# Performance work log

Hardware: AMD Instinct MI355X
Metric: run time of the kernel (lower is better)

Reference implementation:

```python
import jax, jax.numpy as jnp
import numpy as np

NEG_INF = -1e6  # d2l masked_softmax fill value


def setup_inputs() -> dict:
    key = jax.random.key(0)
    kq, kk, kv, kl = jax.random.split(key, 4)
    n, s, d = 32, 2048, 64
    queries = jax.random.normal(kq, (n, s, d), dtype=jnp.float32)
    keys = jax.random.normal(kk, (n, s, d), dtype=jnp.float32)
    values = jax.random.normal(kv, (n, s, d), dtype=jnp.float32)
    valid_lens = jax.random.randint(kl, (n,), 1, s + 1, dtype=jnp.int32)
    return {"queries": queries, "keys": keys, "values": values, "valid_lens": valid_lens}


def reference(queries, keys, values, valid_lens):
    d = queries.shape[-1]
    # scores: [n, q, k]
    scores = jnp.einsum("nqd,nkd->nqk", queries, keys) / jnp.sqrt(jnp.float32(d))
    kv_len = scores.shape[-1]
    # masked_softmax: positions >= valid_len get NEG_INF before softmax
    mask = jnp.arange(kv_len, dtype=jnp.int32)[None, None, :] < valid_lens[:, None, None]
    scores = jnp.where(mask, scores, NEG_INF)
    attn = jax.nn.softmax(scores, axis=-1)
    # dropout rate 0.0 (inference) -> identity
    return jnp.einsum("nqk,nkd->nqd", attn, values)
```

## Files before the change

### kernel.cpp

```cpp
#include <hip/hip_runtime.h>
#include <hip/hip_bf16.h>


typedef short bf16x8 __attribute__((ext_vector_type(8)));
typedef float f32x4  __attribute__((ext_vector_type(4)));
typedef float f32x16 __attribute__((ext_vector_type(16)));
typedef unsigned int u32;
typedef u32 u32x2 __attribute__((ext_vector_type(2)));
typedef u32 u32x4 __attribute__((ext_vector_type(4)));

#define SEQ 2048
#define DH 64
#define BK 64
#define LDSP 72
#define SCLQ 0.18033688011112042f

static __device__ __forceinline__ short f2bf(float f) {
    unsigned u = __float_as_uint(f);
    return (short)((u + 0x7FFFu + ((u >> 16) & 1u)) >> 16);
}
static __device__ __forceinline__ u32 pk2bf(float lo, float hi) {
    __hip_bfloat162 h = __float22bfloat162_rn(float2{lo, hi});
    return *(u32*)&h;
}
static __device__ __forceinline__ void pl32swap(u32& a, u32& b) {
    asm volatile("v_permlane32_swap_b32 %0, %1" : "+v"(a), "+v"(b));
}

__global__ __launch_bounds__(256, 4)
void prepass(const float* __restrict__ K, const float* __restrict__ V,
             short* __restrict__ Kbf, short* __restrict__ Vt)
{
    __shared__ short T[DH][LDSP];

    const int tid  = threadIdx.x;
    const int wave = tid >> 6;
    const int lane = tid & 63;
    const int b  = blockIdx.x & 31;
    const int kt = blockIdx.x >> 5;
    const int k0 = kt * BK;
    const size_t bo = (size_t)b * SEQ * DH;

    const float* Ks = K + bo + (size_t)k0 * DH;
    u32* Kd = (u32*)(Kbf + bo + (size_t)k0 * DH);
    #pragma unroll
    for (int h = 0; h < 2; ++h) {
        const int c2 = tid + h * 256;
        f32x4 a = *(const f32x4*)(Ks + c2 * 8);
        f32x4 c = *(const f32x4*)(Ks + c2 * 8 + 4);
        u32x4 o;
        o[0] = pk2bf(a[0], a[1]); o[1] = pk2bf(a[2], a[3]);
        o[2] = pk2bf(c[0], c[1]); o[3] = pk2bf(c[2], c[3]);
        *(u32x4*)(Kd + c2 * 4) = o;
    }

    #pragma unroll
    for (int h = 0; h < 2; ++h) {
        const int d0 = wave * 8 + h * 32;
        const float* src = V + bo + (size_t)(k0 + lane) * DH + d0;
        f32x4 va = *(const f32x4*)(src);
        f32x4 vb = *(const f32x4*)(src + 4);
        #pragma unroll
        for (int j = 0; j < 4; ++j) {
            T[d0 + j][lane]     = f2bf(va[j]);
            T[d0 + 4 + j][lane] = f2bf(vb[j]);
        }
    }
    __syncthreads();

    short* Vd = Vt + (size_t)b * DH * SEQ;
    #pragma unroll
    for (int h = 0; h < 2; ++h) {
        const int c2 = tid + h * 256;
        const int d  = c2 >> 3;
        const int kc = (c2 & 7) * 8;
        *(bf16x8*)(Vd + (size_t)d * SEQ + k0 + kc) = *(const bf16x8*)(&T[d][kc]);
    }
}

template <bool PRE>
__global__ __launch_bounds__(256, 2)
void attn_fwd(const float* __restrict__ Q,
              const float* __restrict__ Kf, const float* __restrict__ Vf,
              const short* __restrict__ Kbf, const short* __restrict__ Vtg,
              const int* __restrict__ VL, float* __restrict__ O)
{
    __shared__ __align__(16) short Klds[2][BK][LDSP];
    __shared__ __align__(16) short Vt[2][DH][LDSP];
    __shared__ int Rsort[32];

    const int tid  = threadIdx.x;
    const int wave = tid >> 6;
    const int lane = tid & 63;
    const int qg   = wave & 1;
    const int kg   = wave >> 1;
    const int hi   = lane >> 5;
    const int l31  = lane & 31;
    const int pt   = (qg << 6) | lane;

    if (tid < 32) {
        const int nv = (VL[tid] + BK - 1) >> 6;
        int rank = 0;
        for (int jj = 0; jj < 32; ++jj) {
            const int nj = (VL[jj] + BK - 1) >> 6;
            rank += (nj > nv) || (nj == nv && jj < tid);
        }
        Rsort[rank] = tid;
    }
    __syncthreads();

    const int jb = blockIdx.x & 255;
    const int sl = blockIdx.x >> 8;
    const int c8 = jb >> 5;
    const int qt = jb & 31;
    const int rk = (sl == 0) ? c8 : (sl == 1) ? (15 - c8)
                 : (sl == 2) ? (16 + c8) : (31 - c8);
    const int b  = Rsort[rk];

    const int vl   = VL[b];
    const int nkt  = (vl + BK - 1) >> 6;
    const int nkt2 = (nkt + 1) >> 1;

    const size_t bo = (size_t)b * SEQ * DH;
    const short* Kb = Kbf + bo;
    const short* Vb = Vtg + (size_t)b * DH * SEQ;
    const float* Kb32 = Kf + bo;
    const float* Vb32 = Vf + bo;

    const int qrow = qt * 64 + qg * 32 + l31;
    bf16x8 aq[4];
    {
        const float* qp = Q + bo + (size_t)qrow * DH + hi * 8;
        #pragma unroll
        for (int st = 0; st < 4; ++st) {
            f32x4 a = *(const f32x4*)(qp + st * 16);
            f32x4 c = *(const f32x4*)(qp + st * 16 + 4);
            #pragma unroll
            for (int j = 0; j < 4; ++j) {
                aq[st][j]     = f2bf(a[j] * SCLQ);
                aq[st][j + 4] = f2bf(c[j] * SCLQ);
            }
        }
    }

    bf16x8 ones;
    #pragma unroll
    for (int j = 0; j < 8; ++j) ones[j] = (short)0x3F80;

    f32x16 oacc0, oacc1, lacc;
    #pragma unroll
    for (int i = 0; i < 16; ++i) { oacc0[i] = 0.f; oacc1[i] = 0.f; lacc[i] = 0.f; }

    bf16x8 kpre[4], vpre[4];
    if (PRE && kg < nkt) {
        const size_t k0p = (size_t)kg * BK;
        #pragma unroll
        for (int h = 0; h < 4; ++h) {
            const int c = pt + h * 128;
            kpre[h] = *(const bf16x8*)(Kb + k0p * DH + c * 8);
            vpre[h] = *(const bf16x8*)(Vb + (size_t)(c >> 3) * SEQ + k0p + (c & 7) * 8);
        }
    }

    int kt = kg;
    for (int it = 0; it < nkt2; ++it, kt += 2) {
        const bool act = (kt < nkt);
        const int k0 = kt * BK;

        if (act) {
            if (PRE) {
                #pragma unroll
                for (int h = 0; h < 4; ++h) {
                    const int c = pt + h * 128;
                    *(bf16x8*)(&Klds[kg][c >> 3][(c & 7) * 8]) = kpre[h];
                    *(bf16x8*)(&Vt[kg][c >> 3][(c & 7) * 8])   = vpre[h];
                }
            } else {
                #pragma unroll
                for (int h = 0; h < 4; ++h) {
                    const int c = pt + h * 128;
                    const float* ks = Kb32 + (size_t)(k0 + (c >> 3)) * DH + (c & 7) * 8;
                    f32x4 a = *(const f32x4*)ks;
                    f32x4 d = *(const f32x4*)(ks + 4);
                    u32x4 o;
                    o[0] = pk2bf(a[0], a[1]); o[1] = pk2bf(a[2], a[3]);
                    o[2] = pk2bf(d[0], d[1]); o[3] = pk2bf(d[2], d[3]);
                    *(u32x4*)(&Klds[kg][c >> 3][(c & 7) * 8]) = o;
                }
                #pragma unroll
                for (int h = 0; h < 4; ++h) {
                    const int d0 = qg * 32 + h * 8;
                    const float* vs = Vb32 + (size_t)(k0 + lane) * DH + d0;
                    f32x4 a = *(const f32x4*)vs;
                    f32x4 d = *(const f32x4*)(vs + 4);
                    #pragma unroll
                    for (int j = 0; j < 4; ++j) {
                        Vt[kg][d0 + j][lane]     = f2bf(a[j]);
                        Vt[kg][d0 + 4 + j][lane] = f2bf(d[j]);
                    }
                }
            }
        }
        __syncthreads();

        if (PRE && kt + 2 < nkt) {
            const size_t kn = (size_t)(k0 + 2 * BK);
            #pragma unroll
            for (int h = 0; h < 4; ++h) {
                const int c = pt + h * 128;
                kpre[h] = *(const bf16x8*)(Kb + kn * DH + c * 8);
                vpre[h] = *(const bf16x8*)(Vb + (size_t)(c >> 3) * SEQ + kn + (c & 7) * 8);
            }
        }

        if (act) {
            __builtin_amdgcn_s_setprio(1);
            f32x16 s0, s1;
            #pragma unroll
            for (int i = 0; i < 16; ++i) { s0[i] = 0.f; s1[i] = 0.f; }
            #pragma unroll
            for (int st = 0; st < 4; ++st) {
                bf16x8 a0 = *(const bf16x8*)(&Klds[kg][l31][st * 16 + hi * 8]);
                bf16x8 a1 = *(const bf16x8*)(&Klds[kg][32 + l31][st * 16 + hi * 8]);
                s0 = __builtin_amdgcn_mfma_f32_32x32x16_bf16(a0, aq[st], s0, 0, 0, 0);
                s1 = __builtin_amdgcn_mfma_f32_32x32x16_bf16(a1, aq[st], s1, 0, 0, 0);
            }

            if (k0 + BK <= vl) {
                #pragma unroll
                for (int r = 0; r < 16; ++r) {
                    s0[r] = __builtin_amdgcn_exp2f(s0[r]);
                    s1[r] = __builtin_amdgcn_exp2f(s1[r]);
                }
            } else {
                #pragma unroll
                for (int r = 0; r < 16; ++r) {
                    const int krow = k0 + (r & 3) + 8 * (r >> 2) + 4 * hi;
                    s0[r] = (krow < vl)      ? __builtin_amdgcn_exp2f(s0[r]) : 0.f;
                    s1[r] = (krow + 32 < vl) ? __builtin_amdgcn_exp2f(s1[r]) : 0.f;
                }
            }

            u32 pk0[8], pk1[8];
            #pragma unroll
            for (int i = 0; i < 8; ++i) {
                pk0[i] = pk2bf(s0[2 * i], s0[2 * i + 1]);
                pk1[i] = pk2bf(s1[2 * i], s1[2 * i + 1]);
            }

            bf16x8 ap[4];
            #pragma unroll
            for (int t = 0; t < 2; ++t) {
                u32 x0 = pk0[4 * t], x1 = pk0[4 * t + 1];
                u32 x2 = pk0[4 * t + 2], x3 = pk0[4 * t + 3];
                pl32swap(x0, x2); pl32swap(x1, x3);
                u32x4 w; w[0] = x0; w[1] = x1; w[2] = x2; w[3] = x3;
                ap[t] = *(bf16x8*)&w;
                u32 y0 = pk1[4 * t], y1 = pk1[4 * t + 1];
                u32 y2 = pk1[4 * t + 2], y3 = pk1[4 * t + 3];
                pl32swap(y0, y2); pl32swap(y1, y3);
                u32x4 v; v[0] = y0; v[1] = y1; v[2] = y2; v[3] = y3;
                ap[2 + t] = *(bf16x8*)&v;
            }

            #pragma unroll
            for (int ks = 0; ks < 4; ++ks) {
                lacc = __builtin_amdgcn_mfma_f32_32x32x16_bf16(ap[ks], ones, lacc, 0, 0, 0);
                bf16x8 b0 = *(const bf16x8*)(&Vt[kg][l31][ks * 16 + hi * 8]);
                bf16x8 b1 = *(const bf16x8*)(&Vt[kg][32 + l31][ks * 16 + hi * 8]);
                oacc0 = __builtin_amdgcn_mfma_f32_32x32x16_bf16(ap[ks], b0, oacc0, 0, 0, 0);
                oacc1 = __builtin_amdgcn_mfma_f32_32x32x16_bf16(ap[ks], b1, oacc1, 0, 0, 0);
            }
            __builtin_amdgcn_s_setprio(0);
        }
        __syncthreads();
    }

    float* red = (qg ? (float*)&Vt[0][0][0] : (float*)&Klds[0][0][0]) + lane * 52;
    if (kg == 1) {
        *(f32x16*)(red)      = oacc0;
        *(f32x16*)(red + 16) = oacc1;
        *(f32x16*)(red + 32) = lacc;
    }
    __syncthreads();
    if (kg == 0) {
        f32x16 po0 = *(const f32x16*)(red);
        f32x16 po1 = *(const f32x16*)(red + 16);
        f32x16 pl  = *(const f32x16*)(red + 32);
        #pragma unroll
        for (int r = 0; r < 16; ++r) {
            const float inv = 1.0f / (lacc[r] + pl[r]);
            const int row = qt * 64 + qg * 32 + (r & 3) + 8 * (r >> 2) + 4 * hi;
            O[bo + (size_t)row * DH + l31]      = (oacc0[r] + po0[r]) * inv;
            O[bo + (size_t)row * DH + 32 + l31] = (oacc1[r] + po1[r]) * inv;
        }
    }
}

extern "C" void kernel_launch(void* const* d_in, const int* in_sizes, int n_in,
                              void* d_out, int out_size, void* d_ws, size_t ws_size,
                              hipStream_t stream) {
    const float* Q  = (const float*)d_in[0];
    const float* K  = (const float*)d_in[1];
    const float* V  = (const float*)d_in[2];
    const int*   VL = (const int*)d_in[3];
    float* O = (float*)d_out;

    const size_t nel = (size_t)32 * SEQ * DH;
    const size_t need = 2 * nel * sizeof(short);
    if (ws_size >= need) {
        short* Kbf = (short*)d_ws;
        short* Vt  = Kbf + nel;
        prepass<<<dim3(1024), dim3(256), 0, stream>>>(K, V, Kbf, Vt);
        attn_fwd<true><<<dim3(1024), dim3(256), 0, stream>>>(Q, K, V, Kbf, Vt, VL, O);
    } else {
        attn_fwd<false><<<dim3(1024), dim3(256), 0, stream>>>(Q, K, V, nullptr, nullptr, VL, O);
    }
}
```

Baseline: 132.1 us.

## Pre-swizzle K/V into MFMA fragment layout and load directly from global, drop LDS staging

New measurement: 134.7 us. 2.0% more time.

```diff
diff --git a/kernel.cpp b/kernel.cpp
--- a/kernel.cpp
+++ b/kernel.cpp
@@ -6,13 +6,14 @@
 typedef float f32x4  __attribute__((ext_vector_type(4)));
 typedef float f32x16 __attribute__((ext_vector_type(16)));
 typedef unsigned int u32;
-typedef u32 u32x2 __attribute__((ext_vector_type(2)));
 typedef u32 u32x4 __attribute__((ext_vector_type(4)));
 
 #define SEQ 2048
 #define DH 64
 #define BK 64
 #define LDSP 72
+#define FRAG 512
+#define TILE_SH 4096
 #define SCLQ 0.18033688011112042f
 
 static __device__ __forceinline__ short f2bf(float f) {
@@ -29,7 +30,7 @@
 
 __global__ __launch_bounds__(256, 4)
 void prepass(const float* __restrict__ K, const float* __restrict__ V,
-             short* __restrict__ Kbf, short* __restrict__ Vt)
+             short* __restrict__ KF, short* __restrict__ VF)
 {
     __shared__ short T[DH][LDSP];
 
@@ -37,21 +38,25 @@
     const int wave = tid >> 6;
     const int lane = tid & 63;
     const int b  = blockIdx.x & 31;
-    const int kt = blockIdx.x >> 5;
-    const int k0 = kt * BK;
+    const int t  = blockIdx.x >> 5;
+    const int k0 = t * BK;
     const size_t bo = (size_t)b * SEQ * DH;
+    const size_t tb = (size_t)(b * 32 + t) * TILE_SH;
 
     const float* Ks = K + bo + (size_t)k0 * DH;
-    u32* Kd = (u32*)(Kbf + bo + (size_t)k0 * DH);
+    short* Kd = KF + tb;
     #pragma unroll
     for (int h = 0; h < 2; ++h) {
-        const int c2 = tid + h * 256;
-        f32x4 a = *(const f32x4*)(Ks + c2 * 8);
-        f32x4 c = *(const f32x4*)(Ks + c2 * 8 + 4);
+        const int c = tid + h * 256;
+        const int f = c >> 6;
+        const int row = (f & 1) * 32 + (c & 31);
+        const int col = (f >> 1) * 16 + ((c >> 5) & 1) * 8;
+        f32x4 a = *(const f32x4*)(Ks + row * DH + col);
+        f32x4 d = *(const f32x4*)(Ks + row * DH + col + 4);
         u32x4 o;
         o[0] = pk2bf(a[0], a[1]); o[1] = pk2bf(a[2], a[3]);
-        o[2] = pk2bf(c[0], c[1]); o[3] = pk2bf(c[2], c[3]);
-        *(u32x4*)(Kd + c2 * 4) = o;
+        o[2] = pk2bf(d[0], d[1]); o[3] = pk2bf(d[2], d[3]);
+        *(u32x4*)(Kd + c * 8) = o;
     }
 
     #pragma unroll
@@ -68,35 +73,34 @@
     }
     __syncthreads();
 
-    short* Vd = Vt + (size_t)b * DH * SEQ;
+    short* Vd = VF + tb;
     #pragma unroll
     for (int h = 0; h < 2; ++h) {
-        const int c2 = tid + h * 256;
-        const int d  = c2 >> 3;
-        const int kc = (c2 & 7) * 8;
-        *(bf16x8*)(Vd + (size_t)d * SEQ + k0 + kc) = *(const bf16x8*)(&T[d][kc]);
+        const int c = tid + h * 256;
+        const int f = c >> 6;
+        const int trow = (f & 1) * 32 + (c & 31);
+        const int tcol = (f >> 1) * 16 + ((c >> 5) & 1) * 8;
+        *(bf16x8*)(Vd + c * 8) = *(const bf16x8*)(&T[trow][tcol]);
     }
 }
 
 template <bool PRE>
-__global__ __launch_bounds__(256, 2)
+__global__ __launch_bounds__(256, 4)
 void attn_fwd(const float* __restrict__ Q,
               const float* __restrict__ Kf, const float* __restrict__ Vf,
-              const short* __restrict__ Kbf, const short* __restrict__ Vtg,
+              const short* __restrict__ KF, const short* __restrict__ VF,
               const int* __restrict__ VL, float* __restrict__ O)
 {
-    __shared__ __align__(16) short Klds[2][BK][LDSP];
-    __shared__ __align__(16) short Vt[2][DH][LDSP];
+    __shared__ __align__(16) float Red[2][64][44];
     __shared__ int Rsort[32];
 
     const int tid  = threadIdx.x;
     const int wave = tid >> 6;
     const int lane = tid & 63;
     const int qg   = wave & 1;
-    const int kg   = wave >> 1;
+    const int pg   = wave >> 1;
     const int hi   = lane >> 5;
     const int l31  = lane & 31;
-    const int pt   = (qg << 6) | lane;
 
     if (tid < 32) {
         const int nv = (VL[tid] + BK - 1) >> 6;
@@ -115,17 +119,17 @@
     const int qt = jb & 31;
     const int rk = (sl == 0) ? c8 : (sl == 1) ? (15 - c8)
                  : (sl == 2) ? (16 + c8) : (31 - c8);
-    const int b  = Rsort[rk];
-
-    const int vl   = VL[b];
-    const int nkt  = (vl + BK - 1) >> 6;
-    const int nkt2 = (nkt + 1) >> 1;
+    int b = Rsort[rk];
+    b = __builtin_amdgcn_readfirstlane(b);
+
+    const int vl  = __builtin_amdgcn_readfirstlane(VL[b]);
+    const int nkt = (vl + BK - 1) >> 6;
 
     const size_t bo = (size_t)b * SEQ * DH;
-    const short* Kb = Kbf + bo;
-    const short* Vb = Vtg + (size_t)b * DH * SEQ;
-    const float* Kb32 = Kf + bo;
-    const float* Vb32 = Vf + bo;
+    const short* KFb = KF + (size_t)b * 32 * TILE_SH;
+    const short* VFb = VF + (size_t)b * 32 * TILE_SH;
+    const float* Kf32 = Kf + bo;
+    const float* Vf32 = Vf + bo;
 
     const int qrow = qt * 64 + qg * 32 + l31;
     bf16x8 aq[4];
@@ -143,156 +147,154 @@
         }
     }
 
-    bf16x8 ones;
+    f32x16 oacc0, oacc1;
     #pragma unroll
-    for (int j = 0; j < 8; ++j) ones[j] = (short)0x3F80;
-
-    f32x16 oacc0, oacc1, lacc;
-    #pragma unroll
-    for (int i = 0; i < 16; ++i) { oacc0[i] = 0.f; oacc1[i] = 0.f; lacc[i] = 0.f; }
-
-    bf16x8 kpre[4], vpre[4];
-    if (PRE && kg < nkt) {
-        const size_t k0p = (size_t)kg * BK;
-        #pragma unroll
-        for (int h = 0; h < 4; ++h) {
-            const int c = pt + h * 128;
-            kpre[h] = *(const bf16x8*)(Kb + k0p * DH + c * 8);
-            vpre[h] = *(const bf16x8*)(Vb + (size_t)(c >> 3) * SEQ + k0p + (c & 7) * 8);
-        }
-    }
-
-    int kt = kg;
-    for (int it = 0; it < nkt2; ++it, kt += 2) {
-        const bool act = (kt < nkt);
+    for (int i = 0; i < 16; ++i) { oacc0[i] = 0.f; oacc1[i] = 0.f; }
+    float Lrun = 0.f;
+
+    const int lo8 = lane * 8;
+
+    for (int kt = pg; kt < nkt; kt += 2) {
         const int k0 = kt * BK;
-
-        if (act) {
-            if (PRE) {
+        const short* kf = KFb + (size_t)kt * TILE_SH;
+        const short* vf = VFb + (size_t)kt * TILE_SH;
+
+        auto ldA = [&](int f) -> bf16x8 {
+            if constexpr (PRE) {
+                return *(const bf16x8*)(kf + f * FRAG + lo8);
+            } else {
+                const int st = f >> 1, kh = f & 1;
+                const float* p = Kf32 + (size_t)(k0 + kh * 32 + l31) * DH + st * 16 + hi * 8;
+                f32x4 x = *(const f32x4*)p;
+                f32x4 y = *(const f32x4*)(p + 4);
+                bf16x8 r;
                 #pragma unroll
-                for (int h = 0; h < 4; ++h) {
-                    const int c = pt + h * 128;
-                    *(bf16x8*)(&Klds[kg][c >> 3][(c & 7) * 8]) = kpre[h];
-                    *(bf16x8*)(&Vt[kg][c >> 3][(c & 7) * 8])   = vpre[h];
-                }
+                for (int j = 0; j < 4; ++j) { r[j] = f2bf(x[j]); r[j + 4] = f2bf(y[j]); }
+                return r;
+            }
+        };
+        auto ldV = [&](int f) -> bf16x8 {
+            if constexpr (PRE) {
+                return *(const bf16x8*)(vf + f * FRAG + lo8);
             } else {
+                const int ks = f >> 1, dh = f & 1;
+                bf16x8 r;
                 #pragma unroll
-                for (int h = 0; h < 4; ++h) {
-                    const int c = pt + h * 128;
-                    const float* ks = Kb32 + (size_t)(k0 + (c >> 3)) * DH + (c & 7) * 8;
-                    f32x4 a = *(const f32x4*)ks;
-                    f32x4 d = *(const f32x4*)(ks + 4);
-                    u32x4 o;
-                    o[0] = pk2bf(a[0], a[1]); o[1] = pk2bf(a[2], a[3]);
-                    o[2] = pk2bf(d[0], d[1]); o[3] = pk2bf(d[2], d[3]);
-                    *(u32x4*)(&Klds[kg][c >> 3][(c & 7) * 8]) = o;
-                }
-                #pragma unroll
-                for (int h = 0; h < 4; ++h) {
-                    const int d0 = qg * 32 + h * 8;
-                    const float* vs = Vb32 + (size_t)(k0 + lane) * DH + d0;
-                    f32x4 a = *(const f32x4*)vs;
-                    f32x4 d = *(const f32x4*)(vs + 4);
-                    #pragma unroll
-                    for (int j = 0; j < 4; ++j) {
-                        Vt[kg][d0 + j][lane]     = f2bf(a[j]);
-                        Vt[kg][d0 + 4 + j][lane] = f2bf(d[j]);
-                    }
-                }
-            }
-        }
-        __syncthreads();
-
-        if (PRE && kt + 2 < nkt) {
-            const size_t kn = (size_t)(k0 + 2 * BK);
-            #pragma unroll
-            for (int h = 0; h < 4; ++h) {
-                const int c = pt + h * 128;
-                kpre[h] = *(const bf16x8*)(Kb + kn * DH + c * 8);
-                vpre[h] = *(const bf16x8*)(Vb + (size_t)(c >> 3) * SEQ + kn + (c & 7) * 8);
-            }
-        }
-
-        if (act) {
-            __builtin_amdgcn_s_setprio(1);
-            f32x16 s0, s1;
-            #pragma unroll
-            for (int i = 0; i < 16; ++i) { s0[i] = 0.f; s1[i] = 0.f; }
-            #pragma unroll
-            for (int st = 0; st < 4; ++st) {
-                bf16x8 a0 = *(const bf16x8*)(&Klds[kg][l31][st * 16 + hi * 8]);
-                bf16x8 a1 = *(const bf16x8*)(&Klds[kg][32 + l31][st * 16 + hi * 8]);
-                s0 = __builtin_amdgcn_mfma_f32_32x32x16_bf16(a0, aq[st], s0, 0, 0, 0);
-                s1 = __builtin_amdgcn_mfma_f32_32x32x16_bf16(a1, aq[st], s1, 0, 0, 0);
-            }
-
-            if (k0 + BK <= vl) {
-                #pragma unroll
-                for (int r = 0; r < 16; ++r) {
-                    s0[r] = __builtin_amdgcn_exp2f(s0[r]);
-                    s1[r] = __builtin_amdgcn_exp2f(s1[r]);
-                }
-            } else {
-                #pragma unroll
-                for (int r = 0; r < 16; ++r) {
-                    const int krow = k0 + (r & 3) + 8 * (r >> 2) + 4 * hi;
-                    s0[r] = (krow < vl)      ? __builtin_amdgcn_exp2f(s0[r]) : 0.f;
-                    s1[r] = (krow + 32 < vl) ? __builtin_amdgcn_exp2f(s1[r]) : 0.f;
-                }
-            }
-
-            u32 pk0[8], pk1[8];
-            #pragma unroll
-            for (int i = 0; i < 8; ++i) {
-                pk0[i] = pk2bf(s0[2 * i], s0[2 * i + 1]);
-                pk1[i] = pk2bf(s1[2 * i], s1[2 * i + 1]);
-            }
-
-            bf16x8 ap[4];
-            #pragma unroll
-            for (int t = 0; t < 2; ++t) {
-                u32 x0 = pk0[4 * t], x1 = pk0[4 * t + 1];
-                u32 x2 = pk0[4 * t + 2], x3 = pk0[4 * t + 3];
-                pl32swap(x0, x2); pl32swap(x1, x3);
-                u32x4 w; w[0] = x0; w[1] = x1; w[2] = x2; w[3] = x3;
-                ap[t] = *(bf16x8*)&w;
-                u32 y0 = pk1[4 * t], y1 = pk1[4 * t + 1];
-                u32 y2 = pk1[4 * t + 2], y3 = pk1[4 * t + 3];
-                pl32swap(y0, y2); pl32swap(y1, y3);
-                u32x4 v; v[0] = y0; v[1] = y1; v[2] = y2; v[3] = y3;
-                ap[2 + t] = *(bf16x8*)&v;
-            }
-
-            #pragma unroll
-            for (int ks = 0; ks < 4; ++ks) {
-                lacc = __builtin_amdgcn_mfma_f32_32x32x16_bf16(ap[ks], ones, lacc, 0, 0, 0);
-                bf16x8 b0 = *(const bf16x8*)(&Vt[kg][l31][ks * 16 + hi * 8]);
-                bf16x8 b1 = *(const bf16x8*)(&Vt[kg][32 + l31][ks * 16 + hi * 8]);
-                oacc0 = __builtin_amdgcn_mfma_f32_32x32x16_bf16(ap[ks], b0, oacc0, 0, 0, 0);
-                oacc1 = __builtin_amdgcn_mfma_f32_32x32x16_bf16(ap[ks], b1, oacc1, 0, 0, 0);
-            }
-            __builtin_amdgcn_s_setprio(0);
-        }
-        __syncthreads();
-    }
-
-    float* red = (qg ? (float*)&Vt[0][0][0] : (float*)&Klds[0][0][0]) + lane * 52;
-    if (kg == 1) {
-        *(f32x16*)(red)      = oacc0;
-        *(f32x16*)(red + 16) = oacc1;
-        *(f32x16*)(red + 32) = lacc;
+                for (int j = 0; j < 8; ++j)
+                    r[j] = f2bf(Vf32[(size_t)(k0 + ks * 16 + hi * 8 + j) * DH + dh * 32 + l31]);
+                return r;
+            }
+        };
+
+        f32x16 s0, s1;
+        #pragma unroll
+        for (int i = 0; i < 16; ++i) { s0[i] = 0.f; s1[i] = 0.f; }
+
+        __builtin_amdgcn_s_setprio(1);
+        bf16x8 A00 = ldA(0), A01 = ldA(1);
+        bf16x8 A10 = ldA(2), A11 = ldA(3);
+        s0 = __builtin_amdgcn_mfma_f32_32x32x16_bf16(A00, aq[0], s0, 0, 0, 0);
+        s1 = __builtin_amdgcn_mfma_f32_32x32x16_bf16(A01, aq[0], s1, 0, 0, 0);
+        bf16x8 A20 = ldA(4), A21 = ldA(5);
+        s0 = __builtin_amdgcn_mfma_f32_32x32x16_bf16(A10, aq[1], s0, 0, 0, 0);
+        s1 = __builtin_amdgcn_mfma_f32_32x32x16_bf16(A11, aq[1], s1, 0, 0, 0);
+        bf16x8 A30 = ldA(6), A31 = ldA(7);
+        s0 = __builtin_amdgcn_mfma_f32_32x32x16_bf16(A20, aq[2], s0, 0, 0, 0);
+        s1 = __builtin_amdgcn_mfma_f32_32x32x16_bf16(A21, aq[2], s1, 0, 0, 0);
+        s0 = __builtin_amdgcn_mfma_f32_32x32x16_bf16(A30, aq[3], s0, 0, 0, 0);
+        s1 = __builtin_amdgcn_mfma_f32_32x32x16_bf16(A31, aq[3], s1, 0, 0, 0);
+        __builtin_amdgcn_s_setprio(0);
+
+        bf16x8 V00 = ldV(0), V01 = ldV(1);
+        bf16x8 V10 = ldV(2), V11 = ldV(3);
+
+        if (k0 + BK <= vl) {
+            #pragma unroll
+            for (int r = 0; r < 16; ++r) {
+                s0[r] = __builtin_amdgcn_exp2f(s0[r]);
+                s1[r] = __builtin_amdgcn_exp2f(s1[r]);
+            }
+        } else {
+            #pragma unroll
+            for (int r = 0; r < 16; ++r) {
+                const int krow = k0 + (r & 3) + 8 * (r >> 2) + 4 * hi;
+                s0[r] = (krow < vl)      ? __builtin_amdgcn_exp2f(s0[r]) : 0.f;
+                s1[r] = (krow + 32 < vl) ? __builtin_amdgcn_exp2f(s1[r]) : 0.f;
+            }
+        }
+
+        {
+            float ls = 0.f;
+            #pragma unroll
+            for (int r = 0; r < 16; ++r) ls += s0[r] + s1[r];
+            u32 a = __float_as_uint(ls), c = a;
+            pl32swap(a, c);
+            Lrun += __uint_as_float(a) + __uint_as_float(c);
+        }
+
+        u32 pk0[8], pk1[8];
+        #pragma unroll
+        for (int i = 0; i < 8; ++i) {
+            pk0[i] = pk2bf(s0[2 * i], s0[2 * i + 1]);
+            pk1[i] = pk2bf(s1[2 * i], s1[2 * i + 1]);
+        }
+        bf16x8 ap[4];
+        #pragma unroll
+        for (int t = 0; t < 2; ++t) {
+            u32 x0 = pk0[4 * t], x1 = pk0[4 * t + 1];
+            u32 x2 = pk0[4 * t + 2], x3 = pk0[4 * t + 3];
+            pl32swap(x0, x2); pl32swap(x1, x3);
+            u32x4 w; w[0] = x0; w[1] = x1; w[2] = x2; w[3] = x3;
+            ap[t] = *(bf16x8*)&w;
+            u32 y0 = pk1[4 * t], y1 = pk1[4 * t + 1];
+            u32 y2 = pk1[4 * t + 2], y3 = pk1[4 * t + 3];
+            pl32swap(y0, y2); pl32swap(y1, y3);
+            u32x4 v; v[0] = y0; v[1] = y1; v[2] = y2; v[3] = y3;
+            ap[2 + t] = *(bf16x8*)&v;
+        }
+
+        __builtin_amdgcn_s_setprio(1);
+        oacc0 = __builtin_amdgcn_mfma_f32_32x32x16_bf16(ap[0], V00, oacc0, 0, 0, 0);
+        oacc1 = __builtin_amdgcn_mfma_f32_32x32x16_bf16(ap[0], V01, oacc1, 0, 0, 0);
+        bf16x8 V20 = ldV(4), V21 = ldV(5);
+        oacc0 = __builtin_amdgcn_mfma_f32_32x32x16_bf16(ap[1], V10, oacc0, 0, 0, 0);
+        oacc1 = __builtin_amdgcn_mfma_f32_32x32x16_bf16(ap[1], V11, oacc1, 0, 0, 0);
+        bf16x8 V30 = ldV(6), V31 = ldV(7);
+        oacc0 = __builtin_amdgcn_mfma_f32_32x32x16_bf16(ap[2], V20, oacc0, 0, 0, 0);
+        oacc1 = __builtin_amdgcn_mfma_f32_32x32x16_bf16(ap[2], V21, oacc1, 0, 0, 0);
+        oacc0 = __builtin_amdgcn_mfma_f32_32x32x16_bf16(ap[3], V30, oacc0, 0, 0, 0);
+        oacc1 = __builtin_amdgcn_mfma_f32_32x32x16_bf16(ap[3], V31, oacc1, 0, 0, 0);
+        __builtin_amdgcn_s_setprio(0);
+    }
+
+    float* rp = &Red[qg][lane][0];
+    if (pg == 1) {
+        #pragma unroll
+        for (int wd = 0; wd < 4; ++wd) {
+            f32x4 t0, t1;
+            #pragma unroll
+            for (int i = 0; i < 4; ++i) { t0[i] = oacc0[wd * 4 + i]; t1[i] = oacc1[wd * 4 + i]; }
+            *(f32x4*)(rp + wd * 4)      = t0;
+            *(f32x4*)(rp + 16 + wd * 4) = t1;
+        }
+        rp[32] = Lrun;
     }
     __syncthreads();
-    if (kg == 0) {
-        f32x16 po0 = *(const f32x16*)(red);
-        f32x16 po1 = *(const f32x16*)(red + 16);
-        f32x16 pl  = *(const f32x16*)(red + 32);
+    if (pg == 0) {
+        f32x4 p0[4], p1[4];
+        #pragma unroll
+        for (int wd = 0; wd < 4; ++wd) {
+            p0[wd] = *(const f32x4*)(rp + wd * 4);
+            p1[wd] = *(const f32x4*)(rp + 16 + wd * 4);
+        }
+        const float Lq = Lrun + rp[32];
         #pragma unroll
         for (int r = 0; r < 16; ++r) {
-            const float inv = 1.0f / (lacc[r] + pl[r]);
-            const int row = qt * 64 + qg * 32 + (r & 3) + 8 * (r >> 2) + 4 * hi;
-            O[bo + (size_t)row * DH + l31]      = (oacc0[r] + po0[r]) * inv;
-            O[bo + (size_t)row * DH + 32 + l31] = (oacc1[r] + po1[r]) * inv;
+            const int rb = (r & 3) + 8 * (r >> 2) + 4 * hi;
+            const float inv = 1.0f / __shfl(Lq, rb);
+            const int row = qt * 64 + qg * 32 + rb;
+            O[bo + (size_t)row * DH + l31]      = (oacc0[r] + p0[r >> 2][r & 3]) * inv;
+            O[bo + (size_t)row * DH + 32 + l31] = (oacc1[r] + p1[r >> 2][r & 3]) * inv;
         }
     }
 }
@@ -306,13 +308,13 @@
     const int*   VL = (const int*)d_in[3];
     float* O = (float*)d_out;
 
-    const size_t nel = (size_t)32 * SEQ * DH;
+    const size_t nel = (size_t)32 * 32 * TILE_SH;
     const size_t need = 2 * nel * sizeof(short);
     if (ws_size >= need) {
-        short* Kbf = (short*)d_ws;
-        short* Vt  = Kbf + nel;
-        prepass<<<dim3(1024), dim3(256), 0, stream>>>(K, V, Kbf, Vt);
-        attn_fwd<true><<<dim3(1024), dim3(256), 0, stream>>>(Q, K, V, Kbf, Vt, VL, O);
+        short* KF = (short*)d_ws;
+        short* VF = KF + nel;
+        prepass<<<dim3(1024), dim3(256), 0, stream>>>(K, V, KF, VF);
+        attn_fwd<true><<<dim3(1024), dim3(256), 0, stream>>>(Q, K, V, KF, VF, VL, O);
     } else {
         attn_fwd<false><<<dim3(1024), dim3(256), 0, stream>>>(Q, K, V, nullptr, nullptr, VL, O);
     }
```
